# Kernel optimization log

Hardware: AMD Instinct MI355X
Metric: run time of the kernel (lower is better)

The kernel has to match this reference:

```python
import jax, jax.numpy as jnp
import numpy as np

B_, L_, DM, DI, N_, R_ = 8, 2048, 192, 384, 16, 12  # batch, seq, d_model, d_inner, d_state, dt_rank
LN_EPS = 1e-5


def setup_inputs() -> dict:
    key = jax.random.key(0)
    ks = jax.random.split(key, 7)
    x = jax.random.normal(ks[0], (B_, L_, DM), jnp.float32)
    W_in = (jax.random.normal(ks[1], (2 * DI, DM), jnp.float32) * 0.02)
    x_proj_w = (jax.random.normal(ks[2], (R_ + 2 * N_, DI), jnp.float32) * 0.02)
    dt_std = R_ ** (-0.5)
    dt_proj_w = jax.random.uniform(ks[3], (DI, R_), jnp.float32, -dt_std, dt_std)
    # dt bias init: inverse-softplus of dt ~ LogUniform(1e-3, 1e-1)
    dt = jnp.exp(jax.random.uniform(ks[4], (DI,), jnp.float32) * (np.log(0.1) - np.log(0.001)) + np.log(0.001))
    dt = jnp.clip(dt, 1e-4, None)
    dt_proj_b = dt + jnp.log(-jnp.expm1(-dt))
    # A_log init: log(1..N) repeated over d_inner
    A_logs = jnp.log(jnp.tile(jnp.arange(1, N_ + 1, dtype=jnp.float32), (DI, 1)))  # [DI, N]
    Ds = jnp.ones((DI,), jnp.float32)
    ln_gamma = jnp.ones((DI,), jnp.float32)
    ln_beta = jnp.zeros((DI,), jnp.float32)
    W_out = (jax.random.normal(ks[5], (DM, DI), jnp.float32) * 0.02)
    return dict(x=x, W_in=W_in, x_proj_w=x_proj_w, dt_proj_w=dt_proj_w,
                dt_proj_b=dt_proj_b, A_logs=A_logs, Ds=Ds,
                ln_gamma=ln_gamma, ln_beta=ln_beta, W_out=W_out)


def _selective_scan(u, delta, A, Bs, Cs, Ds):
    # u, delta: [B, L, DI]; A: [DI, N]; Bs, Cs: [B, L, N]; Ds: [DI]
    def step(h, inp):
        d_t, u_t, B_t, C_t = inp              # [B,DI], [B,DI], [B,N], [B,N]
        dA = jnp.exp(d_t[..., None] * A)       # [B,DI,N]
        h = dA * h + (d_t * u_t)[..., None] * B_t[:, None, :]
        y_t = jnp.einsum('bdn,bn->bd', h, C_t)
        return h, y_t

    h0 = jnp.zeros((u.shape[0], u.shape[2], A.shape[1]), u.dtype)
    seq = (jnp.moveaxis(delta, 1, 0), jnp.moveaxis(u, 1, 0),
           jnp.moveaxis(Bs, 1, 0), jnp.moveaxis(Cs, 1, 0))
    _, ys = jax.lax.scan(step, h0, seq)        # ys: [L,B,DI]
    return jnp.moveaxis(ys, 0, 1) + Ds * u     # [B,L,DI]


def reference(x, W_in, x_proj_w, dt_proj_w, dt_proj_b, A_logs, Ds, ln_gamma, ln_beta, W_out):
    # in_proj + SiLU, then split into (u, z)  (d_conv <= 1 branch, non-softmax version)
    xz = jax.nn.silu(x @ W_in.T)               # [B,L,2*DI]
    u, z = jnp.split(xz, 2, axis=-1)           # [B,L,DI] each
    # x -> (dt, B, C) projections (K = 1)
    dbl = jnp.einsum('bld,cd->blc', u, x_proj_w)          # [B,L,R+2N]
    dts = dbl[..., :R_] @ dt_proj_w.T                      # [B,L,DI]
    Bs = dbl[..., R_:R_ + N_]                              # [B,L,N]
    Cs = dbl[..., R_ + N_:]                                # [B,L,N]
    delta = jax.nn.softplus(dts + dt_proj_b)               # delta_bias + softplus
    A = -jnp.exp(A_logs)                                   # [DI,N]
    y = _selective_scan(u, delta, A, Bs, Cs, Ds)           # [B,L,DI]
    # out_norm (LayerNorm over d_inner)
    mu = jnp.mean(y, axis=-1, keepdims=True)
    var = jnp.var(y, axis=-1, keepdims=True)
    y = (y - mu) * jax.lax.rsqrt(var + LN_EPS) * ln_gamma + ln_beta
    # gate and out_proj
    y = y * z
    return y @ W_out.T                                     # [B,L,DM]
```

## Files before the change

kernel.cpp:

```cpp
#include <hip/hip_runtime.h>
#include <hip/hip_bf16.h>
#include <math.h>


#define ROWS 16384
#define NCHUNK 64
#define CLEN 32

typedef short bf16x8 __attribute__((ext_vector_type(8)));
typedef float f32x4 __attribute__((ext_vector_type(4)));

__device__ __forceinline__ unsigned short f2bf(float f) {
    unsigned u = __float_as_uint(f);
    return (unsigned short)((u + 0x7fffu + ((u >> 16) & 1u)) >> 16);
}
__device__ __forceinline__ float bf2f(unsigned short h) {
    return __uint_as_float(((unsigned)h) << 16);
}
__device__ __forceinline__ void cvt8(float4 a0, float4 a1, bf16x8& hi, bf16x8& lo) {
    float v[8] = {a0.x, a0.y, a0.z, a0.w, a1.x, a1.y, a1.z, a1.w};
#pragma unroll
    for (int j = 0; j < 8; ++j) {
        unsigned short h = f2bf(v[j]);
        hi[j] = (short)h;
        lo[j] = (short)f2bf(v[j] - bf2f(h));
    }
}

#define LOG2E 1.44269504088896f

__global__ __launch_bounds__(384) void k0_split(
    const float* __restrict__ xpw, short* __restrict__ xpwH, short* __restrict__ xpwL)
{
    const int c = blockIdx.x, k = threadIdx.x;
    float v = (c < 44) ? xpw[(size_t)c * 384 + k] : 0.f;
    unsigned short h = f2bf(v);
    xpwH[(size_t)c * 384 + k] = (short)h;
    xpwL[(size_t)c * 384 + k] = (short)f2bf(v - bf2f(h));
}

#define LDK 40
__global__ __launch_bounds__(256) void k1_gemm_silu(
    const float* __restrict__ x, const float* __restrict__ Win,
    float* __restrict__ u, float* __restrict__ z)
{
    __shared__ short Ah[128 * LDK];
    __shared__ short Al[128 * LDK];
    __shared__ short Bh[128 * LDK];
    __shared__ short Bl[128 * LDK];
    const int tid = threadIdx.x;
    const int lane = tid & 63;
    const int w = tid >> 6;
    const int wr = w >> 1, wc = w & 1;
    const int bm = blockIdx.x * 128;
    const int bn = blockIdx.y * 128;

    f32x4 acc[4][4];
#pragma unroll
    for (int i = 0; i < 4; ++i)
#pragma unroll
        for (int j = 0; j < 4; ++j) acc[i][j] = (f32x4)0.f;

    const int r16 = lane & 15, q4 = lane >> 4;

    for (int k0 = 0; k0 < 192; k0 += 32) {
#pragma unroll
        for (int i = 0; i < 4; ++i) {
            int p = tid + i * 256;
            int r = p >> 3, k4 = (p & 7) * 4;
            float4 av = *(const float4*)(x + (size_t)(bm + r) * 192 + k0 + k4);
            unsigned short hx = f2bf(av.x), hy = f2bf(av.y), hz = f2bf(av.z), hw = f2bf(av.w);
            unsigned hi0 = (unsigned)hx | ((unsigned)hy << 16);
            unsigned hi1 = (unsigned)hz | ((unsigned)hw << 16);
            unsigned short lx = f2bf(av.x - bf2f(hx)), ly = f2bf(av.y - bf2f(hy));
            unsigned short lz = f2bf(av.z - bf2f(hz)), lw = f2bf(av.w - bf2f(hw));
            unsigned lo0 = (unsigned)lx | ((unsigned)ly << 16);
            unsigned lo1 = (unsigned)lz | ((unsigned)lw << 16);
            int wi = r * (LDK / 2) + (k4 >> 1);
            ((unsigned*)Ah)[wi] = hi0; ((unsigned*)Ah)[wi + 1] = hi1;
            ((unsigned*)Al)[wi] = lo0; ((unsigned*)Al)[wi + 1] = lo1;

            float4 bv = *(const float4*)(Win + (size_t)(bn + r) * 192 + k0 + k4);
            hx = f2bf(bv.x); hy = f2bf(bv.y); hz = f2bf(bv.z); hw = f2bf(bv.w);
            hi0 = (unsigned)hx | ((unsigned)hy << 16);
            hi1 = (unsigned)hz | ((unsigned)hw << 16);
            lx = f2bf(bv.x - bf2f(hx)); ly = f2bf(bv.y - bf2f(hy));
            lz = f2bf(bv.z - bf2f(hz)); lw = f2bf(bv.w - bf2f(hw));
            lo0 = (unsigned)lx | ((unsigned)ly << 16);
            lo1 = (unsigned)lz | ((unsigned)lw << 16);
            ((unsigned*)Bh)[wi] = hi0; ((unsigned*)Bh)[wi + 1] = hi1;
            ((unsigned*)Bl)[wi] = lo0; ((unsigned*)Bl)[wi + 1] = lo1;
        }
        __syncthreads();

        bf16x8 ah[4], al[4];
#pragma unroll
        for (int mt = 0; mt < 4; ++mt) {
            int off = (wr * 64 + mt * 16 + r16) * LDK + q4 * 8;
            ah[mt] = *(const bf16x8*)(Ah + off);
            al[mt] = *(const bf16x8*)(Al + off);
        }
#pragma unroll
        for (int nt = 0; nt < 4; ++nt) {
            int off = (wc * 64 + nt * 16 + r16) * LDK + q4 * 8;
            bf16x8 bh = *(const bf16x8*)(Bh + off);
            bf16x8 bl = *(const bf16x8*)(Bl + off);
#pragma unroll
            for (int mt = 0; mt < 4; ++mt) {
                acc[mt][nt] = __builtin_amdgcn_mfma_f32_16x16x32_bf16(ah[mt], bh, acc[mt][nt], 0, 0, 0);
                acc[mt][nt] = __builtin_amdgcn_mfma_f32_16x16x32_bf16(ah[mt], bl, acc[mt][nt], 0, 0, 0);
                acc[mt][nt] = __builtin_amdgcn_mfma_f32_16x16x32_bf16(al[mt], bh, acc[mt][nt], 0, 0, 0);
            }
        }
        __syncthreads();
    }

    float* dst = (bn < 384) ? u : z;
    const int col0 = (bn < 384) ? bn : (bn - 384);
#pragma unroll
    for (int mt = 0; mt < 4; ++mt) {
#pragma unroll
        for (int nt = 0; nt < 4; ++nt) {
            int col = col0 + wc * 64 + nt * 16 + r16;
#pragma unroll
            for (int r = 0; r < 4; ++r) {
                int row = bm + wr * 64 + mt * 16 + q4 * 4 + r;
                float s = acc[mt][nt][r];
                dst[(size_t)row * 384 + col] = s / (1.f + __expf(-s));
            }
        }
    }
}

__global__ __launch_bounds__(384) void k2_proj(
    const float* __restrict__ u, const short* __restrict__ xpwH,
    const short* __restrict__ xpwL,
    const float* __restrict__ dtw, const float* __restrict__ dtb,
    float* __restrict__ delta, float* __restrict__ Bso, float* __restrict__ Cso)
{
    __shared__ float red[2][2][16][49];
    __shared__ float dblS[32 * 13];
    const int tid = threadIdx.x;
    const int lane = tid & 63;
    const int w = tid >> 6;
    const int mt = w & 1, ks = w >> 1;
    const int r16 = lane & 15, q4 = lane >> 4;
    const int row0 = blockIdx.x * 32;
    const int arow = row0 + mt * 16 + r16;

    f32x4 acc[3];
#pragma unroll
    for (int j = 0; j < 3; ++j) acc[j] = (f32x4)0.f;

#pragma unroll
    for (int ck = 0; ck < 4; ++ck) {
        const int kb = ks * 128 + ck * 32 + q4 * 8;
        const float* ap = u + (size_t)arow * 384 + kb;
        float4 a0 = *(const float4*)(ap);
        float4 a1 = *(const float4*)(ap + 4);
        bf16x8 ah, al;
        cvt8(a0, a1, ah, al);
#pragma unroll
        for (int nt = 0; nt < 3; ++nt) {
            const int col = nt * 16 + r16;
            bf16x8 bh = *(const bf16x8*)(xpwH + (size_t)col * 384 + kb);
            bf16x8 bl = *(const bf16x8*)(xpwL + (size_t)col * 384 + kb);
            acc[nt] = __builtin_amdgcn_mfma_f32_16x16x32_bf16(ah, bh, acc[nt], 0, 0, 0);
            acc[nt] = __builtin_amdgcn_mfma_f32_16x16x32_bf16(ah, bl, acc[nt], 0, 0, 0);
            acc[nt] = __builtin_amdgcn_mfma_f32_16x16x32_bf16(al, bh, acc[nt], 0, 0, 0);
        }
    }

    if (ks > 0) {
#pragma unroll
        for (int nt = 0; nt < 3; ++nt)
#pragma unroll
            for (int r = 0; r < 4; ++r)
                red[ks - 1][mt][q4 * 4 + r][nt * 16 + r16] = acc[nt][r];
    }
    __syncthreads();
    if (ks == 0) {
#pragma unroll
        for (int nt = 0; nt < 3; ++nt)
#pragma unroll
            for (int r = 0; r < 4; ++r)
                acc[nt][r] += red[0][mt][q4 * 4 + r][nt * 16 + r16]
                            + red[1][mt][q4 * 4 + r][nt * 16 + r16];

#pragma unroll
        for (int nt = 0; nt < 3; ++nt) {
            int c = nt * 16 + r16;
#pragma unroll
            for (int r = 0; r < 4; ++r) {
                int lr = mt * 16 + q4 * 4 + r;
                int row = row0 + lr;
                float s = acc[nt][r];
                if (c < 12)      dblS[lr * 13 + c] = s;
                else if (c < 28) Bso[(size_t)row * 16 + (c - 12)] = s;
                else if (c < 44) Cso[(size_t)row * 16 + (c - 28)] = s;
            }
        }
    }
    __syncthreads();

    const int d = tid;
    float wr_[12];
#pragma unroll
    for (int j = 0; j < 12; ++j) wr_[j] = dtw[(size_t)d * 12 + j];
    const float bias = dtb[d];
#pragma unroll 4
    for (int r = 0; r < 32; ++r) {
        const float* db = dblS + r * 13;
        float s = bias;
#pragma unroll
        for (int j = 0; j < 12; ++j) s = fmaf(db[j], wr_[j], s);
        float sp = (s > 20.f) ? s : log1pf(__expf(s));
        delta[(size_t)(row0 + r) * 384 + d] = sp;
    }
}

__global__ __launch_bounds__(384) void k3a_scan1(
    const float* __restrict__ delta, const float* __restrict__ u,
    const float* __restrict__ Bsv, const float* __restrict__ A_logs,
    float* __restrict__ hf, float* __restrict__ Ssum)
{
    const int tid = threadIdx.x;
    const int lane = tid & 63;
    const int wv = tid >> 6;
    const int c = blockIdx.x;
    const int b = blockIdx.y;
    const int d = wv * 64 + lane;
    const int t0 = c * CLEN;

    float Ac[16];
    {
#pragma unroll
        for (int q = 0; q < 4; ++q) {
            float4 v = *(const float4*)(A_logs + d * 16 + q * 4);
            Ac[q * 4 + 0] = -__expf(v.x) * LOG2E;
            Ac[q * 4 + 1] = -__expf(v.y) * LOG2E;
            Ac[q * 4 + 2] = -__expf(v.z) * LOG2E;
            Ac[q * 4 + 3] = -__expf(v.w) * LOG2E;
        }
    }

    const float* dp = delta + ((size_t)b * 2048 + t0) * 384 + d;
    const float* up = u     + ((size_t)b * 2048 + t0) * 384 + d;
    const float* Bp = Bsv   + ((size_t)b * 2048 + t0) * 16;

    float h[16];
#pragma unroll
    for (int n = 0; n < 16; ++n) h[n] = 0.f;
    float S = 0.f;

    float dv_n = dp[0], uv_n = up[0];
    float4 B0n = *(const float4*)(Bp + 0);
    float4 B1n = *(const float4*)(Bp + 4);
    float4 B2n = *(const float4*)(Bp + 8);
    float4 B3n = *(const float4*)(Bp + 12);

    for (int s = 0; s < CLEN; ++s) {
        float dv = dv_n, uv = uv_n;
        float4 B0 = B0n, B1 = B1n, B2 = B2n, B3 = B3n;
        if (s + 1 < CLEN) {
            dp += 384; up += 384; Bp += 16;
            dv_n = dp[0]; uv_n = up[0];
            B0n = *(const float4*)(Bp + 0);
            B1n = *(const float4*)(Bp + 4);
            B2n = *(const float4*)(Bp + 8);
            B3n = *(const float4*)(Bp + 12);
        }
        __builtin_amdgcn_sched_barrier(0);
        S += dv;
        float dvu = dv * uv;
        float Br[16] = {B0.x, B0.y, B0.z, B0.w, B1.x, B1.y, B1.z, B1.w,
                        B2.x, B2.y, B2.z, B2.w, B3.x, B3.y, B3.z, B3.w};
#pragma unroll
        for (int n = 0; n < 16; ++n) {
            float a = exp2f(dv * Ac[n]);
            h[n] = fmaf(a, h[n], dvu * Br[n]);
        }
    }

    const size_t ho = (((size_t)b * NCHUNK + c) * 384 + d) * 16;
#pragma unroll
    for (int q = 0; q < 4; ++q)
        *(float4*)(hf + ho + q * 4) = make_float4(h[q*4+0], h[q*4+1], h[q*4+2], h[q*4+3]);
    Ssum[((size_t)b * NCHUNK + c) * 384 + d] = S;
}

__global__ __launch_bounds__(256) void k3c_combine(
    float* __restrict__ hf, const float* __restrict__ Ssum,
    const float* __restrict__ A_logs)
{
    const int tid = threadIdx.x;
    const int n = tid & 15, dl = tid >> 4;
    const int d = blockIdx.x * 16 + dl;
    const int b = blockIdx.y;
    const float Ac = -__expf(A_logs[d * 16 + n]) * LOG2E;

    float h = 0.f;
    for (int c = 0; c < NCHUNK; ++c) {
        const size_t idx = (((size_t)b * NCHUNK + c) * 384 + d) * 16 + n;
        float hfv = hf[idx];
        float Sv  = Ssum[((size_t)b * NCHUNK + c) * 384 + d];
        hf[idx] = h;
        float P = exp2f(Ac * Sv);
        h = fmaf(P, h, hfv);
    }
}

__global__ __launch_bounds__(384) void k3b_scan2(
    float* __restrict__ dy, const float* __restrict__ u,
    const float* __restrict__ Bsv, const float* __restrict__ Csv,
    const float* __restrict__ A_logs, const float* __restrict__ Ds,
    const float* __restrict__ hf)
{
    const int tid = threadIdx.x;
    const int lane = tid & 63;
    const int wv = tid >> 6;
    const int c = blockIdx.x;
    const int b = blockIdx.y;
    const int d = wv * 64 + lane;
    const int t0 = c * CLEN;

    float Ac[16];
#pragma unroll
    for (int q = 0; q < 4; ++q) {
        float4 v = *(const float4*)(A_logs + d * 16 + q * 4);
        Ac[q * 4 + 0] = -__expf(v.x) * LOG2E;
        Ac[q * 4 + 1] = -__expf(v.y) * LOG2E;
        Ac[q * 4 + 2] = -__expf(v.z) * LOG2E;
        Ac[q * 4 + 3] = -__expf(v.w) * LOG2E;
    }
    const float Dd = Ds[d];

    float h[16];
    {
        const size_t ho = (((size_t)b * NCHUNK + c) * 384 + d) * 16;
#pragma unroll
        for (int q = 0; q < 4; ++q) {
            float4 v = *(const float4*)(hf + ho + q * 4);
            h[q * 4 + 0] = v.x; h[q * 4 + 1] = v.y;
            h[q * 4 + 2] = v.z; h[q * 4 + 3] = v.w;
        }
    }

    float* yp       = dy  + ((size_t)b * 2048 + t0) * 384 + d;
    const float* up = u   + ((size_t)b * 2048 + t0) * 384 + d;
    const float* Bp = Bsv + ((size_t)b * 2048 + t0) * 16;
    const float* Cp = Csv + ((size_t)b * 2048 + t0) * 16;

    float dv_n = yp[0], uv_n = up[0];
    float4 B0n = *(const float4*)(Bp + 0);
    float4 B1n = *(const float4*)(Bp + 4);
    float4 B2n = *(const float4*)(Bp + 8);
    float4 B3n = *(const float4*)(Bp + 12);
    float4 C0n = *(const float4*)(Cp + 0);
    float4 C1n = *(const float4*)(Cp + 4);
    float4 C2n = *(const float4*)(Cp + 8);
    float4 C3n = *(const float4*)(Cp + 12);
    const float* dpn = yp + 384;

    for (int s = 0; s < CLEN; ++s) {
        float dv = dv_n, uv = uv_n;
        float4 B0 = B0n, B1 = B1n, B2 = B2n, B3 = B3n;
        float4 C0 = C0n, C1 = C1n, C2 = C2n, C3 = C3n;
        if (s + 1 < CLEN) {
            up += 384; Bp += 16; Cp += 16;
            dv_n = dpn[0]; uv_n = up[0];
            B0n = *(const float4*)(Bp + 0);
            B1n = *(const float4*)(Bp + 4);
            B2n = *(const float4*)(Bp + 8);
            B3n = *(const float4*)(Bp + 12);
            C0n = *(const float4*)(Cp + 0);
            C1n = *(const float4*)(Cp + 4);
            C2n = *(const float4*)(Cp + 8);
            C3n = *(const float4*)(Cp + 12);
            dpn += 384;
        }
        __builtin_amdgcn_sched_barrier(0);
        float dvu = dv * uv;
        float Br[16] = {B0.x, B0.y, B0.z, B0.w, B1.x, B1.y, B1.z, B1.w,
                        B2.x, B2.y, B2.z, B2.w, B3.x, B3.y, B3.z, B3.w};
        float Cr[16] = {C0.x, C0.y, C0.z, C0.w, C1.x, C1.y, C1.z, C1.w,
                        C2.x, C2.y, C2.z, C2.w, C3.x, C3.y, C3.z, C3.w};
        float y = Dd * uv;
#pragma unroll
        for (int n = 0; n < 16; ++n) {
            float a = exp2f(dv * Ac[n]);
            h[n] = fmaf(a, h[n], dvu * Br[n]);
            y = fmaf(Cr[n], h[n], y);
        }
        yp[0] = y;
        yp += 384;
    }
}

__global__ __launch_bounds__(256) void k4_ln_mul(
    float* __restrict__ y, const float* __restrict__ z,
    const float* __restrict__ gamma, const float* __restrict__ beta)
{
    const int tid = threadIdx.x;
    const int lane = tid & 63;
    const int w = tid >> 6;
    const size_t row = (size_t)blockIdx.x * 4 + w;
    float* yr = y + row * 384;
    const float* zr = z + row * 384;
    float v[6];
    float s1 = 0.f, s2 = 0.f;
#pragma unroll
    for (int j = 0; j < 6; ++j) {
        v[j] = yr[lane + j * 64];
        s1 += v[j];
        s2 = fmaf(v[j], v[j], s2);
    }
#pragma unroll
    for (int off = 32; off > 0; off >>= 1) {
        s1 += __shfl_xor(s1, off);
        s2 += __shfl_xor(s2, off);
    }
    float mu = s1 * (1.f / 384.f);
    float var = s2 * (1.f / 384.f) - mu * mu;
    float rs = rsqrtf(var + 1e-5f);
#pragma unroll
    for (int j = 0; j < 6; ++j) {
        int d = lane + j * 64;
        float o = (v[j] - mu) * rs * gamma[d] + beta[d];
        yr[d] = o * zr[d];
    }
}

__global__ __launch_bounds__(256) void k5_gemm_out(
    const float* __restrict__ yn, const float* __restrict__ Wout,
    float* __restrict__ out)
{
    __shared__ short Ah[128 * LDK];
    __shared__ short Al[128 * LDK];
    __shared__ short Bh[64 * LDK];
    __shared__ short Bl[64 * LDK];
    const int tid = threadIdx.x;
    const int lane = tid & 63;
    const int w = tid >> 6;
    const int wr = w >> 1, wc = w & 1;
    const int bm = blockIdx.x * 128;
    const int bn = blockIdx.y * 64;

    f32x4 acc[4][2];
#pragma unroll
    for (int i = 0; i < 4; ++i)
#pragma unroll
        for (int j = 0; j < 2; ++j) acc[i][j] = (f32x4)0.f;

    const int r16 = lane & 15, q4 = lane >> 4;

    for (int k0 = 0; k0 < 384; k0 += 32) {
#pragma unroll
        for (int i = 0; i < 4; ++i) {
            int p = tid + i * 256;
            int r = p >> 3, k4 = (p & 7) * 4;
            float4 av = *(const float4*)(yn + (size_t)(bm + r) * 384 + k0 + k4);
            unsigned short hx = f2bf(av.x), hy = f2bf(av.y), hz = f2bf(av.z), hw = f2bf(av.w);
            unsigned hi0 = (unsigned)hx | ((unsigned)hy << 16);
            unsigned hi1 = (unsigned)hz | ((unsigned)hw << 16);
            unsigned short lx = f2bf(av.x - bf2f(hx)), ly = f2bf(av.y - bf2f(hy));
            unsigned short lz = f2bf(av.z - bf2f(hz)), lw = f2bf(av.w - bf2f(hw));
            unsigned lo0 = (unsigned)lx | ((unsigned)ly << 16);
            unsigned lo1 = (unsigned)lz | ((unsigned)lw << 16);
            int wi = r * (LDK / 2) + (k4 >> 1);
            ((unsigned*)Ah)[wi] = hi0; ((unsigned*)Ah)[wi + 1] = hi1;
            ((unsigned*)Al)[wi] = lo0; ((unsigned*)Al)[wi + 1] = lo1;
        }
#pragma unroll
        for (int i = 0; i < 2; ++i) {
            int p = tid + i * 256;
            int r = p >> 3, k4 = (p & 7) * 4;
            float4 bv = *(const float4*)(Wout + (size_t)(bn + r) * 384 + k0 + k4);
            unsigned short hx = f2bf(bv.x), hy = f2bf(bv.y), hz = f2bf(bv.z), hw = f2bf(bv.w);
            unsigned hi0 = (unsigned)hx | ((unsigned)hy << 16);
            unsigned hi1 = (unsigned)hz | ((unsigned)hw << 16);
            unsigned short lx = f2bf(bv.x - bf2f(hx)), ly = f2bf(bv.y - bf2f(hy));
            unsigned short lz = f2bf(bv.z - bf2f(hz)), lw = f2bf(bv.w - bf2f(hw));
            unsigned lo0 = (unsigned)lx | ((unsigned)ly << 16);
            unsigned lo1 = (unsigned)lz | ((unsigned)lw << 16);
            int wi = r * (LDK / 2) + (k4 >> 1);
            ((unsigned*)Bh)[wi] = hi0; ((unsigned*)Bh)[wi + 1] = hi1;
            ((unsigned*)Bl)[wi] = lo0; ((unsigned*)Bl)[wi + 1] = lo1;
        }
        __syncthreads();

        bf16x8 ah[4], al[4];
#pragma unroll
        for (int mt = 0; mt < 4; ++mt) {
            int off = (wr * 64 + mt * 16 + r16) * LDK + q4 * 8;
            ah[mt] = *(const bf16x8*)(Ah + off);
            al[mt] = *(const bf16x8*)(Al + off);
        }
#pragma unroll
        for (int nt = 0; nt < 2; ++nt) {
            int off = (wc * 32 + nt * 16 + r16) * LDK + q4 * 8;
            bf16x8 bh = *(const bf16x8*)(Bh + off);
            bf16x8 bl = *(const bf16x8*)(Bl + off);
#pragma unroll
            for (int mt = 0; mt < 4; ++mt) {
                acc[mt][nt] = __builtin_amdgcn_mfma_f32_16x16x32_bf16(ah[mt], bh, acc[mt][nt], 0, 0, 0);
                acc[mt][nt] = __builtin_amdgcn_mfma_f32_16x16x32_bf16(ah[mt], bl, acc[mt][nt], 0, 0, 0);
                acc[mt][nt] = __builtin_amdgcn_mfma_f32_16x16x32_bf16(al[mt], bh, acc[mt][nt], 0, 0, 0);
            }
        }
        __syncthreads();
    }

#pragma unroll
    for (int mt = 0; mt < 4; ++mt) {
#pragma unroll
        for (int nt = 0; nt < 2; ++nt) {
            int col = bn + wc * 32 + nt * 16 + r16;
#pragma unroll
            for (int r = 0; r < 4; ++r) {
                int row = bm + wr * 64 + mt * 16 + q4 * 4 + r;
                out[(size_t)row * 192 + col] = acc[mt][nt][r];
            }
        }
    }
}

extern "C" void kernel_launch(void* const* d_in, const int* in_sizes, int n_in,
                              void* d_out, int out_size, void* d_ws, size_t ws_size,
                              hipStream_t stream) {
    const float* x    = (const float*)d_in[0];
    const float* Win  = (const float*)d_in[1];
    const float* xpw  = (const float*)d_in[2];
    const float* dtw  = (const float*)d_in[3];
    const float* dtb  = (const float*)d_in[4];
    const float* Alog = (const float*)d_in[5];
    const float* Dsv  = (const float*)d_in[6];
    const float* lng  = (const float*)d_in[7];
    const float* lnb  = (const float*)d_in[8];
    const float* Wout = (const float*)d_in[9];
    float* out = (float*)d_out;

    const size_t nU  = (size_t)ROWS * 384;
    const size_t nBC = (size_t)ROWS * 16;
    const size_t nHF = (size_t)8 * NCHUNK * 384 * 16;
    const size_t nS  = (size_t)8 * NCHUNK * 384;
    const size_t nXW = (size_t)48 * 384;
    const size_t need = (nU * 3 + nBC * 2 + nHF + nS) * sizeof(float) + nXW * 2 * sizeof(short);
    if (ws_size < need) return;

    float* u    = (float*)d_ws;
    float* z    = u + nU;
    float* dl   = z + nU;
    float* Bsv  = dl + nU;
    float* Csv  = Bsv + nBC;
    float* hf   = Csv + nBC;
    float* Ssum = hf + nHF;
    short* xpwH = (short*)(Ssum + nS);
    short* xpwL = xpwH + nXW;

    k0_split<<<48, 384, 0, stream>>>(xpw, xpwH, xpwL);
    k1_gemm_silu<<<dim3(128, 6), 256, 0, stream>>>(x, Win, u, z);
    k2_proj<<<512, 384, 0, stream>>>(u, xpwH, xpwL, dtw, dtb, dl, Bsv, Csv);
    k3a_scan1<<<dim3(NCHUNK, 8), 384, 0, stream>>>(dl, u, Bsv, Alog, hf, Ssum);
    k3c_combine<<<dim3(24, 8), 256, 0, stream>>>(hf, Ssum, Alog);
    k3b_scan2<<<dim3(NCHUNK, 8), 384, 0, stream>>>(dl, u, Bsv, Csv, Alog, Dsv, hf);
    k4_ln_mul<<<4096, 256, 0, stream>>>(dl, z, lng, lnb);
    k5_gemm_out<<<dim3(128, 3), 256, 0, stream>>>(dl, Wout, out);
}
```

Baseline: 276.6 us.

## Fuse LayerNorm and gating into scan pass two, halve chunk length

Moves the LayerNorm+gate step into the second scan kernel. Each block stages its chunk's outputs in shared memory and normalizes rows there, so the separate k4 launch and its round trip of y through global memory go away. Chunk count doubles to 128 and chunk length halves to 16, which gives more blocks for parallelism and keeps the shared buffer small. The cost is more chunk states to write and combine, and a serial combine that runs twice as many steps.

Result: faster. 257.0 us (-7.1%).

```diff
diff --git a/kernel.cpp b/kernel.cpp
--- a/kernel.cpp
+++ b/kernel.cpp
@@ -4,8 +4,8 @@
 
 
 #define ROWS 16384
-#define NCHUNK 64
-#define CLEN 32
+#define NCHUNK 128
+#define CLEN 16
 
 typedef short bf16x8 __attribute__((ext_vector_type(8)));
 typedef float f32x4 __attribute__((ext_vector_type(4)));
@@ -314,8 +314,10 @@
     float* __restrict__ dy, const float* __restrict__ u,
     const float* __restrict__ Bsv, const float* __restrict__ Csv,
     const float* __restrict__ A_logs, const float* __restrict__ Ds,
-    const float* __restrict__ hf)
-{
+    const float* __restrict__ hf, const float* __restrict__ zbuf,
+    const float* __restrict__ gamma, const float* __restrict__ beta)
+{
+    __shared__ float yS[CLEN * 384];
     const int tid = threadIdx.x;
     const int lane = tid & 63;
     const int wv = tid >> 6;
@@ -346,12 +348,12 @@
         }
     }
 
-    float* yp       = dy  + ((size_t)b * 2048 + t0) * 384 + d;
+    const float* dp = dy  + ((size_t)b * 2048 + t0) * 384 + d;
     const float* up = u   + ((size_t)b * 2048 + t0) * 384 + d;
     const float* Bp = Bsv + ((size_t)b * 2048 + t0) * 16;
     const float* Cp = Csv + ((size_t)b * 2048 + t0) * 16;
 
-    float dv_n = yp[0], uv_n = up[0];
+    float dv_n = dp[0], uv_n = up[0];
     float4 B0n = *(const float4*)(Bp + 0);
     float4 B1n = *(const float4*)(Bp + 4);
     float4 B2n = *(const float4*)(Bp + 8);
@@ -360,15 +362,14 @@
     float4 C1n = *(const float4*)(Cp + 4);
     float4 C2n = *(const float4*)(Cp + 8);
     float4 C3n = *(const float4*)(Cp + 12);
-    const float* dpn = yp + 384;
 
     for (int s = 0; s < CLEN; ++s) {
         float dv = dv_n, uv = uv_n;
         float4 B0 = B0n, B1 = B1n, B2 = B2n, B3 = B3n;
         float4 C0 = C0n, C1 = C1n, C2 = C2n, C3 = C3n;
         if (s + 1 < CLEN) {
-            up += 384; Bp += 16; Cp += 16;
-            dv_n = dpn[0]; uv_n = up[0];
+            dp += 384; up += 384; Bp += 16; Cp += 16;
+            dv_n = dp[0]; uv_n = up[0];
             B0n = *(const float4*)(Bp + 0);
             B1n = *(const float4*)(Bp + 4);
             B2n = *(const float4*)(Bp + 8);
@@ -377,7 +378,6 @@
             C1n = *(const float4*)(Cp + 4);
             C2n = *(const float4*)(Cp + 8);
             C3n = *(const float4*)(Cp + 12);
-            dpn += 384;
         }
         __builtin_amdgcn_sched_barrier(0);
         float dvu = dv * uv;
@@ -392,42 +392,37 @@
             h[n] = fmaf(a, h[n], dvu * Br[n]);
             y = fmaf(Cr[n], h[n], y);
         }
-        yp[0] = y;
-        yp += 384;
-    }
-}
-
-__global__ __launch_bounds__(256) void k4_ln_mul(
-    float* __restrict__ y, const float* __restrict__ z,
-    const float* __restrict__ gamma, const float* __restrict__ beta)
-{
-    const int tid = threadIdx.x;
-    const int lane = tid & 63;
-    const int w = tid >> 6;
-    const size_t row = (size_t)blockIdx.x * 4 + w;
-    float* yr = y + row * 384;
-    const float* zr = z + row * 384;
-    float v[6];
-    float s1 = 0.f, s2 = 0.f;
-#pragma unroll
-    for (int j = 0; j < 6; ++j) {
-        v[j] = yr[lane + j * 64];
-        s1 += v[j];
-        s2 = fmaf(v[j], v[j], s2);
-    }
-#pragma unroll
-    for (int off = 32; off > 0; off >>= 1) {
-        s1 += __shfl_xor(s1, off);
-        s2 += __shfl_xor(s2, off);
-    }
-    float mu = s1 * (1.f / 384.f);
-    float var = s2 * (1.f / 384.f) - mu * mu;
-    float rs = rsqrtf(var + 1e-5f);
-#pragma unroll
-    for (int j = 0; j < 6; ++j) {
-        int d = lane + j * 64;
-        float o = (v[j] - mu) * rs * gamma[d] + beta[d];
-        yr[d] = o * zr[d];
+        yS[s * 384 + d] = y;
+    }
+    __syncthreads();
+
+    for (int r = wv; r < CLEN; r += 6) {
+        const float* ys = yS + r * 384;
+        float v[6];
+        float s1 = 0.f, s2 = 0.f;
+#pragma unroll
+        for (int j = 0; j < 6; ++j) {
+            v[j] = ys[j * 64 + lane];
+            s1 += v[j];
+            s2 = fmaf(v[j], v[j], s2);
+        }
+#pragma unroll
+        for (int off = 32; off > 0; off >>= 1) {
+            s1 += __shfl_xor(s1, off);
+            s2 += __shfl_xor(s2, off);
+        }
+        float mu = s1 * (1.f / 384.f);
+        float var = s2 * (1.f / 384.f) - mu * mu;
+        float rs = rsqrtf(var + 1e-5f);
+        const size_t row = (size_t)b * 2048 + t0 + r;
+        float* yr = dy + row * 384;
+        const float* zr = zbuf + row * 384;
+#pragma unroll
+        for (int j = 0; j < 6; ++j) {
+            int dd = j * 64 + lane;
+            float o = (v[j] - mu) * rs * gamma[dd] + beta[dd];
+            yr[dd] = o * zr[dd];
+        }
     }
 }
 
@@ -563,7 +558,6 @@
     k2_proj<<<512, 384, 0, stream>>>(u, xpwH, xpwL, dtw, dtb, dl, Bsv, Csv);
     k3a_scan1<<<dim3(NCHUNK, 8), 384, 0, stream>>>(dl, u, Bsv, Alog, hf, Ssum);
     k3c_combine<<<dim3(24, 8), 256, 0, stream>>>(hf, Ssum, Alog);
-    k3b_scan2<<<dim3(NCHUNK, 8), 384, 0, stream>>>(dl, u, Bsv, Csv, Alog, Dsv, hf);
-    k4_ln_mul<<<4096, 256, 0, stream>>>(dl, z, lng, lnb);
+    k3b_scan2<<<dim3(NCHUNK, 8), 384, 0, stream>>>(dl, u, Bsv, Csv, Alog, Dsv, hf, z, lng, lnb);
     k5_gemm_out<<<dim3(128, 3), 256, 0, stream>>>(dl, Wout, out);
 }
```
